# Performance work log

Measured on AMD Instinct MI355X. Metric: run time of the kernel, lower is better.

## Reference

```python
import jax, jax.numpy as jnp
import numpy as np

N, E = 50000, 300000
IN, HID, OUT, HEADS = 768, 256, 128, 8
RELS = ("writes", "written_by", "cites")


def setup_inputs():
    ks = iter(jax.random.split(jax.random.key(0), 64))

    def nrm(shape, scale=1.0):
        return jax.random.normal(next(ks), shape, dtype=jnp.float32) * scale

    inp = {"x_paper": nrm((N, IN)), "x_author": nrm((N, IN))}
    for name in ("ei_writes", "ei_written_by", "ei_cites"):
        inp[name] = jax.random.randint(next(ks), (2, E), 0, N, dtype=jnp.int32)
    # layer 0: in=IN, out=HID, heads=HEADS
    s0 = 1.0 / np.sqrt(IN)
    inp["W0_paper"] = nrm((IN, HID), s0); inp["b0_paper"] = jnp.zeros((HID,), jnp.float32)
    inp["W0_author"] = nrm((IN, HID), s0); inp["b0_author"] = jnp.zeros((HID,), jnp.float32)
    D0 = HID // HEADS
    for rel in RELS:
        inp["a0s_" + rel] = nrm((HEADS, D0), 0.1)
        inp["a0d_" + rel] = nrm((HEADS, D0), 0.1)
    inp["Wk0"] = nrm((HID, HID), 1.0 / np.sqrt(HID)); inp["bk0"] = jnp.zeros((HID,), jnp.float32)
    inp["q0"] = nrm((HID,), 0.1)
    # layer 1 (last): in=HID, out=OUT, heads=1
    s1 = 1.0 / np.sqrt(HID)
    inp["W1_paper"] = nrm((HID, OUT), s1); inp["b1_paper"] = jnp.zeros((OUT,), jnp.float32)
    inp["W1_author"] = nrm((HID, OUT), s1); inp["b1_author"] = jnp.zeros((OUT,), jnp.float32)
    for rel in RELS:
        inp["a1s_" + rel] = nrm((1, OUT), 0.1)
        inp["a1d_" + rel] = nrm((1, OUT), 0.1)
    inp["Wk1"] = nrm((OUT, OUT), 1.0 / np.sqrt(OUT)); inp["bk1"] = jnp.zeros((OUT,), jnp.float32)
    inp["q1"] = nrm((OUT,), 0.1)
    return inp


def _han_layer(xs, proj, att, Wk, bk, q, edges, heads):
    # xs: {ntype: [N, in]}, proj: {ntype: (W, b)}, att: {rel: (a_src[H,D], a_dst[H,D])}
    C = q.shape[0]
    D = C // heads
    xh = {nt: (x @ proj[nt][0] + proj[nt][1]).reshape(-1, heads, D) for nt, x in xs.items()}
    outs = {nt: [] for nt in xs}
    for (st, rel, dt), ei in edges:
        a_s, a_d = att[rel]
        xsrc, xdst = xh[st], xh[dt]
        src, dst = ei[0], ei[1]
        n = xdst.shape[0]
        # GAT-style edge scores per head: [E, H]
        al = jax.nn.leaky_relu((xsrc * a_s).sum(-1)[src] + (xdst * a_d).sum(-1)[dst], 0.2)
        amax = jax.lax.stop_gradient(jax.ops.segment_max(al, dst, num_segments=n))
        ex = jnp.exp(al - amax[dst])
        alpha = ex / (jax.ops.segment_sum(ex, dst, num_segments=n)[dst] + 1e-16)
        msg = xsrc[src] * alpha[:, :, None]                      # [E, H, D]
        agg = jax.ops.segment_sum(msg, dst, num_segments=n)      # [n, H, D]
        outs[dt].append(jax.nn.relu(agg.reshape(n, C)))
    # semantic attention across metapaths (group)
    res = {}
    for nt, lst in outs.items():
        stk = jnp.stack(lst)                                     # [M, n, C]
        score = (q * jnp.tanh(stk @ Wk + bk).mean(axis=1)).sum(-1)
        w = jax.nn.softmax(score)                                # [M]
        res[nt] = jnp.einsum('m,mnc->nc', w, stk)
    return res


def reference(x_paper, x_author, W0_paper, b0_paper, W0_author, b0_author,
              a0s_writes, a0d_writes, a0s_written_by, a0d_written_by, a0s_cites, a0d_cites,
              Wk0, bk0, q0,
              W1_paper, b1_paper, W1_author, b1_author,
              a1s_writes, a1d_writes, a1s_written_by, a1d_written_by, a1s_cites, a1d_cites,
              Wk1, bk1, q1,
              ei_writes, ei_written_by, ei_cites):
    edges = [(("author", "writes", "paper"), ei_writes),
             (("paper", "written_by", "author"), ei_written_by),
             (("paper", "cites", "paper"), ei_cites)]
    h = _han_layer({"paper": x_paper, "author": x_author},
                   {"paper": (W0_paper, b0_paper), "author": (W0_author, b0_author)},
                   {"writes": (a0s_writes, a0d_writes),
                    "written_by": (a0s_written_by, a0d_written_by),
                    "cites": (a0s_cites, a0d_cites)},
                   Wk0, bk0, q0, edges, HEADS)
    h = {k: jax.nn.elu(v) for k, v in h.items()}
    h = _han_layer(h,
                   {"paper": (W1_paper, b1_paper), "author": (W1_author, b1_author)},
                   {"writes": (a1s_writes, a1d_writes),
                    "written_by": (a1s_written_by, a1d_written_by),
                    "cites": (a1s_cites, a1d_cites)},
                   Wk1, bk1, q1, edges, 1)

    def l2n(v):
        return v / jnp.maximum(jnp.linalg.norm(v, axis=1, keepdims=True), 1e-12)

    return (l2n(h["paper"]), l2n(h["author"]))
```

## Files before the change

### kernel.cpp

```cpp
#include <hip/hip_runtime.h>
#include <math.h>

#define NN 50000
#define NE 300000
#define DIN 768
#define DHID 256
#define DOUT 128
#define H0 8
#define D0 32
#define OFFST (NN + 4)

typedef __attribute__((ext_vector_type(8))) short bf16x8;
typedef __attribute__((ext_vector_type(8))) unsigned short u16x8;
typedef __attribute__((ext_vector_type(4))) float f32x4;

__device__ __forceinline__ unsigned short f2bf(float f) {
    unsigned u = __float_as_uint(f);
    unsigned r = (u + 0x7fffu + ((u >> 16) & 1u)) >> 16;
    return (unsigned short)r;
}
__device__ __forceinline__ float bf2f(unsigned short u) {
    return __uint_as_float(((unsigned)u) << 16);
}

__device__ __forceinline__ void gload16(const void* g, void* l) {
    __builtin_amdgcn_global_load_lds(
        (const __attribute__((address_space(1))) unsigned int*)g,
        (__attribute__((address_space(3))) unsigned int*)l, 16, 0, 0);
}

__device__ __forceinline__ void store_bf8(unsigned short* dst, float4 lo, float4 hi) {
    u16x8 o;
    o[0] = f2bf(lo.x); o[1] = f2bf(lo.y); o[2] = f2bf(lo.z); o[3] = f2bf(lo.w);
    o[4] = f2bf(hi.x); o[5] = f2bf(hi.y); o[6] = f2bf(hi.z); o[7] = f2bf(hi.w);
    *(u16x8*)dst = o;
}

__global__ void transconv3_kernel(const float* __restrict__ Wa, const float* __restrict__ Wb,
                                  const float* __restrict__ Wc,
                                  unsigned short* __restrict__ Ta, unsigned short* __restrict__ Tb,
                                  unsigned short* __restrict__ Tc,
                                  int Kab, int Nab, int Kc, int Ncc)
{
    int y = blockIdx.y;
    const float* W = (y == 0) ? Wa : ((y == 1) ? Wb : Wc);
    unsigned short* T = (y == 0) ? Ta : ((y == 1) ? Tb : Tc);
    int K = (y == 2) ? Kc : Kab;
    int Nc = (y == 2) ? Ncc : Nab;
    int gid = blockIdx.x * 256 + threadIdx.x;
    if (gid >= K * Nc) return;
    int k = gid / Nc, n = gid - k * Nc;
    T[(size_t)n * K + k] = f2bf(W[gid]);
}

__global__ __launch_bounds__(512) void gemm_l0_kernel(
    const float* __restrict__ A0, const float* __restrict__ A1,
    const unsigned short* __restrict__ Bt0, const unsigned short* __restrict__ Bt1,
    const float* __restrict__ bias0, const float* __restrict__ bias1,
    unsigned short* __restrict__ C0, unsigned short* __restrict__ C1)
{
    constexpr int K  = DIN;
    constexpr int Nc = DHID;
    constexpr int NT = K / 32;
    __shared__ __align__(16) unsigned short As[2][128 * 32];
    __shared__ __align__(16) unsigned short Bs[2][256 * 32];
    const int z = blockIdx.y;
    const float* A = z ? A1 : A0;
    const unsigned short* Bt = z ? Bt1 : Bt0;
    const float* bias = z ? bias1 : bias0;
    unsigned short* C = z ? C1 : C0;
    const int t = threadIdx.x;
    const int lane = t & 63, w = t >> 6;
    const int wr = w >> 2, wc = w & 3;
    const int bm = blockIdx.x * 128;

    f32x4 acc[4][4];
    #pragma unroll
    for (int m = 0; m < 4; ++m)
        #pragma unroll
        for (int n = 0; n < 4; ++n)
            acc[m][n] = (f32x4){0.f, 0.f, 0.f, 0.f};

    const int arow = t >> 2;
    const int ags = (t & 3) ^ ((arow >> 1) & 3);
    int ar = bm + arow; if (ar >= NN) ar = NN - 1;
    const float* pA = A + (size_t)ar * K + ags * 8;
    const int b0row = t >> 2;
    const int bg0 = (t & 3) ^ ((b0row >> 1) & 3);
    const unsigned short* pB0 = Bt + (size_t)b0row * K + bg0 * 8;
    const int c1i = t + 512;
    const int b1row = c1i >> 2;
    const int bg1 = (c1i & 3) ^ ((b1row >> 1) & 3);
    const unsigned short* pB1 = Bt + (size_t)b1row * K + bg1 * 8;

    const int rA = wr * 64 + (lane & 15);
    const int rB = wc * 64 + (lane & 15);
    const int gw = lane >> 4;

    float4 ra[2][2];
    {
        float4 t0 = *(const float4*)(pA);
        float4 t1 = *(const float4*)(pA + 4);
        gload16(pB0, &Bs[0][(size_t)t * 8]);
        gload16(pB1, &Bs[0][(size_t)c1i * 8]);
        ra[1][0] = *(const float4*)(pA + 32);
        ra[1][1] = *(const float4*)(pA + 36);
        gload16(pB0 + 32, &Bs[1][(size_t)t * 8]);
        gload16(pB1 + 32, &Bs[1][(size_t)c1i * 8]);
        store_bf8(&As[0][(size_t)t * 8], t0, t1);
    }
    asm volatile("s_waitcnt vmcnt(4) lgkmcnt(0)\n\ts_barrier" ::: "memory");

    #pragma unroll
    for (int ti = 0; ti < NT; ++ti) {
        const int cur = ti & 1;
        const int nxt = cur ^ 1;
        if (ti + 1 < NT) {
            const int nk = (ti + 1) * 32;
            gload16(pB0 + nk, &Bs[nxt][(size_t)t * 8]);
            gload16(pB1 + nk, &Bs[nxt][(size_t)c1i * 8]);
        }
        if (ti + 2 < NT) {
            const int nk = (ti + 2) * 32;
            ra[cur][0] = *(const float4*)(pA + nk);
            ra[cur][1] = *(const float4*)(pA + nk + 4);
        }
        bf16x8 afr[4], bfr[4];
        #pragma unroll
        for (int m = 0; m < 4; ++m) {
            int r = rA + m * 16;
            afr[m] = *(const bf16x8*)&As[cur][r * 32 + ((gw ^ ((r >> 1) & 3)) * 8)];
        }
        #pragma unroll
        for (int n = 0; n < 4; ++n) {
            int r = rB + n * 16;
            bfr[n] = *(const bf16x8*)&Bs[cur][r * 32 + ((gw ^ ((r >> 1) & 3)) * 8)];
        }
        #pragma unroll
        for (int m = 0; m < 4; ++m)
            #pragma unroll
            for (int n = 0; n < 4; ++n)
                acc[m][n] = __builtin_amdgcn_mfma_f32_16x16x32_bf16(afr[m], bfr[n], acc[m][n], 0, 0, 0);
        if (ti + 1 < NT) {
            store_bf8(&As[nxt][(size_t)t * 8], ra[nxt][0], ra[nxt][1]);
            if (ti + 2 < NT) asm volatile("s_waitcnt vmcnt(2) lgkmcnt(0)\n\ts_barrier" ::: "memory");
            else             asm volatile("s_waitcnt vmcnt(0) lgkmcnt(0)\n\ts_barrier" ::: "memory");
        }
    }

    #pragma unroll
    for (int m = 0; m < 4; ++m) {
        #pragma unroll
        for (int j = 0; j < 4; ++j) {
            int row = bm + wr * 64 + m * 16 + (lane >> 4) * 4 + j;
            if (row >= NN) continue;
            #pragma unroll
            for (int n = 0; n < 4; ++n) {
                int col = wc * 64 + n * 16 + (lane & 15);
                C[(size_t)row * Nc + col] = f2bf(acc[m][n][j] + bias[col]);
            }
        }
    }
}

__global__ __launch_bounds__(256) void gemm_bf16_kernel(
    const unsigned short* __restrict__ A0, const unsigned short* __restrict__ A1,
    const unsigned short* __restrict__ Bt0, const unsigned short* __restrict__ Bt1,
    const float* __restrict__ bias0, const float* __restrict__ bias1,
    unsigned short* __restrict__ C0, unsigned short* __restrict__ C1,
    int M, int K, int Nc)
{
    __shared__ __align__(16) unsigned short As[2][128 * 32];
    __shared__ __align__(16) unsigned short Bs[2][128 * 32];
    const int z = blockIdx.z;
    const unsigned short* A  = z ? A1  : A0;
    const unsigned short* Bt = z ? Bt1 : Bt0;
    const float* bias = z ? bias1 : bias0;
    unsigned short* C = z ? C1 : C0;
    const int t = threadIdx.x;
    const int lane = t & 63, w = t >> 6;
    const int wr = w >> 1, wc = w & 1;
    const int bm = blockIdx.y * 128, bn = blockIdx.x * 128;

    f32x4 acc[4][4];
    #pragma unroll
    for (int m = 0; m < 4; ++m)
        #pragma unroll
        for (int n = 0; n < 4; ++n)
            acc[m][n] = (f32x4){0.f, 0.f, 0.f, 0.f};

    const int c0 = w * 64 + lane, c1 = c0 + 256;
    const int row0 = c0 >> 2, row1 = c1 >> 2;
    const int g0 = (c0 & 3) ^ ((row0 >> 1) & 3);
    const int g1 = (c1 & 3) ^ ((row1 >> 1) & 3);
    const int ar0 = (bm + row0 < M) ? (bm + row0) : (M - 1);
    const int ar1 = (bm + row1 < M) ? (bm + row1) : (M - 1);
    const unsigned short* pA0 = A + (size_t)ar0 * K + g0 * 8;
    const unsigned short* pA1 = A + (size_t)ar1 * K + g1 * 8;
    const unsigned short* pB0 = Bt + (size_t)(bn + row0) * K + g0 * 8;
    const unsigned short* pB1 = Bt + (size_t)(bn + row1) * K + g1 * 8;

    const int rA = wr * 64 + (lane & 15);
    const int rB = wc * 64 + (lane & 15);
    const int gw = lane >> 4;
    const int nt = K >> 5;

    gload16(pA0, &As[0][c0 * 8]);
    gload16(pA1, &As[0][c1 * 8]);
    gload16(pB0, &Bs[0][c0 * 8]);
    gload16(pB1, &Bs[0][c1 * 8]);
    __syncthreads();
    for (int ti = 0; ti < nt; ++ti) {
        const int cur = ti & 1;
        if (ti + 1 < nt) {
            const int nk = (ti + 1) << 5;
            const int nb = cur ^ 1;
            gload16(pA0 + nk, &As[nb][c0 * 8]);
            gload16(pA1 + nk, &As[nb][c1 * 8]);
            gload16(pB0 + nk, &Bs[nb][c0 * 8]);
            gload16(pB1 + nk, &Bs[nb][c1 * 8]);
        }
        bf16x8 afr[4], bfr[4];
        #pragma unroll
        for (int m = 0; m < 4; ++m) {
            int r = rA + m * 16;
            afr[m] = *(const bf16x8*)&As[cur][r * 32 + ((gw ^ ((r >> 1) & 3)) * 8)];
        }
        #pragma unroll
        for (int n = 0; n < 4; ++n) {
            int r = rB + n * 16;
            bfr[n] = *(const bf16x8*)&Bs[cur][r * 32 + ((gw ^ ((r >> 1) & 3)) * 8)];
        }
        #pragma unroll
        for (int m = 0; m < 4; ++m)
            #pragma unroll
            for (int n = 0; n < 4; ++n)
                acc[m][n] = __builtin_amdgcn_mfma_f32_16x16x32_bf16(afr[m], bfr[n], acc[m][n], 0, 0, 0);
        __syncthreads();
    }
    #pragma unroll
    for (int m = 0; m < 4; ++m) {
        #pragma unroll
        for (int j = 0; j < 4; ++j) {
            int row = bm + wr * 64 + m * 16 + (lane >> 4) * 4 + j;
            if (row >= M) continue;
            #pragma unroll
            for (int n = 0; n < 4; ++n) {
                int col = bn + wc * 64 + n * 16 + (lane & 15);
                C[(size_t)row * Nc + col] = f2bf(acc[m][n][j] + bias[col]);
            }
        }
    }
}

__global__ __launch_bounds__(256) void sem2_bf16_kernel(
    const unsigned short* __restrict__ Aa, const unsigned short* __restrict__ Ab,
    const unsigned short* __restrict__ Bt,
    const float* __restrict__ bk, float* __restrict__ partial0,
    int M, int K, int Nc)
{
    __shared__ __align__(16) unsigned short As[2][128 * 32];
    __shared__ __align__(16) unsigned short Bs[2][128 * 32];
    __shared__ float red[128];
    const int z = blockIdx.z;
    const unsigned short* A = z ? Ab : Aa;
    float* partial = partial0 + z * Nc;
    const int t = threadIdx.x;
    const int lane = t & 63, w = t >> 6;
    const int wr = w >> 1, wc = w & 1;
    const int bm = blockIdx.y * 128, bn = blockIdx.x * 128;

    f32x4 acc[4][4];
    #pragma unroll
    for (int m = 0; m < 4; ++m)
        #pragma unroll
        for (int n = 0; n < 4; ++n)
            acc[m][n] = (f32x4){0.f, 0.f, 0.f, 0.f};

    const int c0 = w * 64 + lane, c1 = c0 + 256;
    const int row0 = c0 >> 2, row1 = c1 >> 2;
    const int g0 = (c0 & 3) ^ ((row0 >> 1) & 3);
    const int g1 = (c1 & 3) ^ ((row1 >> 1) & 3);
    const int ar0 = (bm + row0 < M) ? (bm + row0) : (M - 1);
    const int ar1 = (bm + row1 < M) ? (bm + row1) : (M - 1);
    const unsigned short* pA0 = A + (size_t)ar0 * K + g0 * 8;
    const unsigned short* pA1 = A + (size_t)ar1 * K + g1 * 8;
    const unsigned short* pB0 = Bt + (size_t)(bn + row0) * K + g0 * 8;
    const unsigned short* pB1 = Bt + (size_t)(bn + row1) * K + g1 * 8;

    const int rA = wr * 64 + (lane & 15);
    const int rB = wc * 64 + (lane & 15);
    const int gw = lane >> 4;
    const int nt = K >> 5;

    gload16(pA0, &As[0][c0 * 8]);
    gload16(pA1, &As[0][c1 * 8]);
    gload16(pB0, &Bs[0][c0 * 8]);
    gload16(pB1, &Bs[0][c1 * 8]);
    __syncthreads();
    for (int ti = 0; ti < nt; ++ti) {
        const int cur = ti & 1;
        if (ti + 1 < nt) {
            const int nk = (ti + 1) << 5;
            const int nb = cur ^ 1;
            gload16(pA0 + nk, &As[nb][c0 * 8]);
            gload16(pA1 + nk, &As[nb][c1 * 8]);
            gload16(pB0 + nk, &Bs[nb][c0 * 8]);
            gload16(pB1 + nk, &Bs[nb][c1 * 8]);
        }
        bf16x8 afr[4], bfr[4];
        #pragma unroll
        for (int m = 0; m < 4; ++m) {
            int r = rA + m * 16;
            afr[m] = *(const bf16x8*)&As[cur][r * 32 + ((gw ^ ((r >> 1) & 3)) * 8)];
        }
        #pragma unroll
        for (int n = 0; n < 4; ++n) {
            int r = rB + n * 16;
            bfr[n] = *(const bf16x8*)&Bs[cur][r * 32 + ((gw ^ ((r >> 1) & 3)) * 8)];
        }
        #pragma unroll
        for (int m = 0; m < 4; ++m)
            #pragma unroll
            for (int n = 0; n < 4; ++n)
                acc[m][n] = __builtin_amdgcn_mfma_f32_16x16x32_bf16(afr[m], bfr[n], acc[m][n], 0, 0, 0);
        __syncthreads();
    }
    if (t < 128) red[t] = 0.f;
    __syncthreads();
    #pragma unroll
    for (int n = 0; n < 4; ++n) {
        int lcol = wc * 64 + n * 16 + (lane & 15);
        float b = bk[bn + lcol];
        float s = 0.f;
        #pragma unroll
        for (int m = 0; m < 4; ++m) {
            #pragma unroll
            for (int j = 0; j < 4; ++j) {
                int row = bm + wr * 64 + m * 16 + (lane >> 4) * 4 + j;
                if (row < M) s += tanhf(acc[m][n][j] + b);
            }
        }
        atomicAdd(&red[lcol], s);
    }
    __syncthreads();
    if (t < 128) atomicAdd(&partial[bn + t], red[t]);
}

__global__ void hist3_kernel(const int* __restrict__ d0, const int* __restrict__ d1,
                             const int* __restrict__ d2, int* __restrict__ deg3)
{
    int gid = blockIdx.x * 256 + threadIdx.x;
    if (gid >= 3 * NE) return;
    int rel = gid / NE, e = gid - rel * NE;
    const int* dst = (rel == 0) ? d0 : ((rel == 1) ? d1 : d2);
    atomicAdd(&deg3[rel * NN + dst[e]], 1);
}

__global__ void block_sum3_kernel(const int* __restrict__ deg3, int* __restrict__ bsum3)
{
    __shared__ int buf[256];
    int rel = blockIdx.y;
    int i = blockIdx.x * 256 + threadIdx.x;
    buf[threadIdx.x] = (i < NN) ? deg3[rel * NN + i] : 0;
    __syncthreads();
    for (int s = 128; s > 0; s >>= 1) {
        if (threadIdx.x < s) buf[threadIdx.x] += buf[threadIdx.x + s];
        __syncthreads();
    }
    if (threadIdx.x == 0) bsum3[rel * 256 + blockIdx.x] = buf[0];
}

__global__ void scan_bsum3_kernel(const int* __restrict__ bsum3, int* __restrict__ boff3, int nb)
{
    __shared__ int buf[256];
    int rel = blockIdx.y;
    int tid = threadIdx.x;
    int v = (tid < nb) ? bsum3[rel * 256 + tid] : 0;
    buf[tid] = v;
    __syncthreads();
    for (int off = 1; off < 256; off <<= 1) {
        int t = (tid >= off) ? buf[tid - off] : 0;
        __syncthreads();
        buf[tid] += t;
        __syncthreads();
    }
    if (tid < nb) boff3[rel * 256 + tid] = buf[tid] - v;
}

__global__ void scan_final3_kernel(const int* __restrict__ deg3, const int* __restrict__ boff3,
                                   int* __restrict__ offs3)
{
    __shared__ int buf[256];
    int rel = blockIdx.y;
    int tid = threadIdx.x, b = blockIdx.x;
    int i = b * 256 + tid;
    int v = (i < NN) ? deg3[rel * NN + i] : 0;
    buf[tid] = v;
    __syncthreads();
    for (int off = 1; off < 256; off <<= 1) {
        int t = (tid >= off) ? buf[tid - off] : 0;
        __syncthreads();
        buf[tid] += t;
        __syncthreads();
    }
    int* offs = offs3 + rel * OFFST;
    if (i < NN) offs[i] = boff3[rel * 256 + b] + buf[tid] - v;
    if (i == NN - 1) offs[NN] = boff3[rel * 256 + b] + buf[tid];
}

__global__ void place3_kernel(const int* __restrict__ s0, const int* __restrict__ s1,
                              const int* __restrict__ s2,
                              const int* __restrict__ offs3, int* __restrict__ cnt3,
                              int* __restrict__ esrc3)
{
    int rel = blockIdx.y;
    int e = blockIdx.x * 256 + threadIdx.x;
    if (e >= NE) return;
    const int* srcdst = (rel == 0) ? s0 : ((rel == 1) ? s1 : s2);
    int src = srcdst[e];
    int d = srcdst[NE + e];
    int p = offs3[rel * OFFST + d] + atomicAdd(&cnt3[rel * NN + d], 1);
    esrc3[rel * NE + p] = src;
}

__global__ void scores_L0_kernel(
    const unsigned short* __restrict__ xp, const unsigned short* __restrict__ xa,
    const float* __restrict__ a_dw, const float* __restrict__ a_swb,
    const float* __restrict__ a_sc, const float* __restrict__ a_dc,
    const float* __restrict__ a_sw, const float* __restrict__ a_dwb,
    float* __restrict__ sW_dst, float* __restrict__ sWB_src,
    float* __restrict__ sC_src, float* __restrict__ sC_dst,
    float* __restrict__ sW_src, float* __restrict__ sWB_dst)
{
    int gid = blockIdx.x * 256 + threadIdx.x;
    int half = NN * H0;
    if (gid >= 2 * half) return;
    if (gid < half) {
        int node = gid >> 3, h = gid & 7;
        const unsigned short* xr = xp + (size_t)node * DHID + h * D0;
        float xv[D0];
        #pragma unroll
        for (int j = 0; j < 4; ++j) {
            u16x8 v = ((const u16x8*)xr)[j];
            #pragma unroll
            for (int k = 0; k < 8; ++k) xv[j * 8 + k] = bf2f(v[k]);
        }
        const float* p0 = a_dw  + h * D0;
        const float* p1 = a_swb + h * D0;
        const float* p2 = a_sc  + h * D0;
        const float* p3 = a_dc  + h * D0;
        float d0 = 0.f, d1 = 0.f, d2 = 0.f, d3 = 0.f;
        #pragma unroll
        for (int k = 0; k < D0; ++k) {
            float x = xv[k];
            d0 += x * p0[k]; d1 += x * p1[k]; d2 += x * p2[k]; d3 += x * p3[k];
        }
        sW_dst[gid] = d0; sWB_src[gid] = d1; sC_src[gid] = d2; sC_dst[gid] = d3;
    } else {
        int g = gid - half;
        int node = g >> 3, h = g & 7;
        const unsigned short* xr = xa + (size_t)node * DHID + h * D0;
        float xv[D0];
        #pragma unroll
        for (int j = 0; j < 4; ++j) {
            u16x8 v = ((const u16x8*)xr)[j];
            #pragma unroll
            for (int k = 0; k < 8; ++k) xv[j * 8 + k] = bf2f(v[k]);
        }
        const float* p0 = a_sw  + h * D0;
        const float* p1 = a_dwb + h * D0;
        float d0 = 0.f, d1 = 0.f;
        #pragma unroll
        for (int k = 0; k < D0; ++k) {
            float x = xv[k];
            d0 += x * p0[k]; d1 += x * p1[k];
        }
        sW_src[g] = d0; sWB_dst[g] = d1;
    }
}

__global__ void scores_L1_kernel(
    const unsigned short* __restrict__ xp, const unsigned short* __restrict__ xa,
    const float* __restrict__ a_dw, const float* __restrict__ a_swb,
    const float* __restrict__ a_sc, const float* __restrict__ a_dc,
    const float* __restrict__ a_sw, const float* __restrict__ a_dwb,
    float* __restrict__ sW_dst, float* __restrict__ sWB_src,
    float* __restrict__ sC_src, float* __restrict__ sC_dst,
    float* __restrict__ sW_src, float* __restrict__ sWB_dst)
{
    int gid = blockIdx.x * 256 + threadIdx.x;
    if (gid >= 2 * NN) return;
    if (gid < NN) {
        const unsigned short* xr = xp + (size_t)gid * DOUT;
        float d0 = 0.f, d1 = 0.f, d2 = 0.f, d3 = 0.f;
        for (int j = 0; j < DOUT / 8; ++j) {
            u16x8 v = ((const u16x8*)xr)[j];
            #pragma unroll
            for (int k = 0; k < 8; ++k) {
                float x = bf2f(v[k]);
                int c = j * 8 + k;
                d0 += x * a_dw[c]; d1 += x * a_swb[c]; d2 += x * a_sc[c]; d3 += x * a_dc[c];
            }
        }
        sW_dst[gid] = d0; sWB_src[gid] = d1; sC_src[gid] = d2; sC_dst[gid] = d3;
    } else {
        int g = gid - NN;
        const unsigned short* xr = xa + (size_t)g * DOUT;
        float d0 = 0.f, d1 = 0.f;
        for (int j = 0; j < DOUT / 8; ++j) {
            u16x8 v = ((const u16x8*)xr)[j];
            #pragma unroll
            for (int k = 0; k < 8; ++k) {
                float x = bf2f(v[k]);
                int c = j * 8 + k;
                d0 += x * a_sw[c]; d1 += x * a_dwb[c];
            }
        }
        sW_src[g] = d0; sWB_dst[g] = d1;
    }
}

__global__ void seg_alpha3_kernel(
    const int* __restrict__ offs3, const int* __restrict__ esrc3,
    const float* __restrict__ ss0, const float* __restrict__ ss1, const float* __restrict__ ss2,
    const float* __restrict__ sd0, const float* __restrict__ sd1, const float* __restrict__ sd2,
    float* __restrict__ alpha3, int H)
{
    int rel = blockIdx.y;
    const int* offs = offs3 + rel * OFFST;
    const int* esrc = esrc3 + rel * NE;
    const float* ssrc = (rel == 0) ? ss0 : ((rel == 1) ? ss1 : ss2);
    const float* sdst = (rel == 0) ? sd0 : ((rel == 1) ? sd1 : sd2);
    float* alpha = alpha3 + (size_t)rel * NE * H0;
    int gid = blockIdx.x * 256 + threadIdx.x;
    if (gid >= NN * H) return;
    int d = gid / H, h = gid - d * H;
    int beg = offs[d], end = offs[d + 1];
    float sd = sdst[gid];
    float m = -INFINITY, den = 0.f;
    for (int i = beg; i < end; ++i) {
        int s = esrc[i];
        float v = ssrc[s * H + h] + sd;
        v = (v >= 0.f) ? v : 0.2f * v;
        if (v > m) { den = den * expf(m - v) + 1.f; m = v; }
        else       den += expf(v - m);
    }
    float inv = 1.f / (den + 1e-16f);
    for (int i = beg; i < end; ++i) {
        int s = esrc[i];
        float v = ssrc[s * H + h] + sd;
        v = (v >= 0.f) ? v : 0.2f * v;
        alpha[(size_t)i * H + h] = expf(v - m) * inv;
    }
}

template<int CPL, int HH, int DSH>
__global__ __launch_bounds__(256) void gather3_kernel(
    const int* __restrict__ offs3, const int* __restrict__ esrc3,
    const float* __restrict__ alpha3,
    const unsigned short* __restrict__ x0, const unsigned short* __restrict__ x1,
    const unsigned short* __restrict__ x2,
    unsigned short* __restrict__ o0, unsigned short* __restrict__ o1,
    unsigned short* __restrict__ o2, int C)
{
    int rel = blockIdx.y;
    const int* offs = offs3 + rel * OFFST;
    const int* esrc = esrc3 + rel * NE;
    const float* alpha = alpha3 + (size_t)rel * NE * H0;
    const unsigned short* x = (rel == 0) ? x0 : ((rel == 1) ? x1 : x2);
    unsigned short* outp = (rel == 0) ? o0 : ((rel == 1) ? o1 : o2);

    int wid = threadIdx.x >> 6, lane = threadIdx.x & 63;
    int d = blockIdx.x * 4 + wid;
    int c0 = lane * CPL;
    int h = c0 >> DSH;
    int beg = offs[d], end = offs[d + 1];
    float acc0 = 0.f, acc1 = 0.f, acc2 = 0.f, acc3 = 0.f;
    int n = end - beg;
    if (n > 0) {
        int sA = esrc[beg];
        float aA = alpha[(size_t)beg * HH + h];
        int sB = sA; float aB = 0.f;
        if (n > 1) { sB = esrc[beg + 1]; aB = alpha[(size_t)(beg + 1) * HH + h]; }
        if (CPL == 4) {
            ushort4 xc = *(const ushort4*)(x + (size_t)sA * C + c0);
            for (int i = beg; i < end; ++i) {
                ushort4 xn = xc;
                if (i + 1 < end) xn = *(const ushort4*)(x + (size_t)sB * C + c0);
                int sN = sB; float aN = 0.f;
                if (i + 2 < end) { sN = esrc[i + 2]; aN = alpha[(size_t)(i + 2) * HH + h]; }
                acc0 += aA * bf2f(xc.x); acc1 += aA * bf2f(xc.y);
                acc2 += aA * bf2f(xc.z); acc3 += aA * bf2f(xc.w);
                xc = xn; aA = aB; sB = sN; aB = aN;
            }
        } else {
            ushort2 xc = *(const ushort2*)(x + (size_t)sA * C + c0);
            for (int i = beg; i < end; ++i) {
                ushort2 xn = xc;
                if (i + 1 < end) xn = *(const ushort2*)(x + (size_t)sB * C + c0);
                int sN = sB; float aN = 0.f;
                if (i + 2 < end) { sN = esrc[i + 2]; aN = alpha[(size_t)(i + 2) * HH + h]; }
                acc0 += aA * bf2f(xc.x); acc1 += aA * bf2f(xc.y);
                xc = xn; aA = aB; sB = sN; aB = aN;
            }
        }
    }
    unsigned short* op = outp + (size_t)d * C + c0;
    if (CPL == 4) {
        ushort4 st;
        st.x = f2bf(fmaxf(acc0, 0.f)); st.y = f2bf(fmaxf(acc1, 0.f));
        st.z = f2bf(fmaxf(acc2, 0.f)); st.w = f2bf(fmaxf(acc3, 0.f));
        *(ushort4*)op = st;
    } else {
        ushort2 st;
        st.x = f2bf(fmaxf(acc0, 0.f)); st.y = f2bf(fmaxf(acc1, 0.f));
        *(ushort2*)op = st;
    }
}

__global__ void sem_weights_kernel(const float* __restrict__ partial, const float* __restrict__ q,
                                   float* __restrict__ w, int C, int n)
{
    if (threadIdx.x != 0 || blockIdx.x != 0) return;
    float inv = 1.f / (float)n;
    float s0 = 0.f, s1 = 0.f;
    for (int c = 0; c < C; ++c) {
        s0 += q[c] * partial[c] * inv;
        s1 += q[c] * partial[C + c] * inv;
    }
    float m = fmaxf(s0, s1);
    float e0 = expf(s0 - m), e1 = expf(s1 - m);
    float den = e0 + e1;
    w[0] = e0 / den;
    w[1] = e1 / den;
}

__global__ void combine2_bf16_kernel(const unsigned short* __restrict__ a,
                                     const unsigned short* __restrict__ b,
                                     const float* __restrict__ w, unsigned short* __restrict__ out,
                                     int n8)
{
    int i = blockIdx.x * 256 + threadIdx.x;
    if (i >= n8) return;
    float w0 = w[0], w1 = w[1];
    u16x8 va = ((const u16x8*)a)[i];
    u16x8 vb = ((const u16x8*)b)[i];
    u16x8 o;
    #pragma unroll
    for (int j = 0; j < 8; ++j) o[j] = f2bf(w0 * bf2f(va[j]) + w1 * bf2f(vb[j]));
    ((u16x8*)out)[i] = o;
}

__global__ __launch_bounds__(128) void final_norm_kernel(
    const unsigned short* __restrict__ aggW, const unsigned short* __restrict__ aggC,
    const unsigned short* __restrict__ aggB, const float* __restrict__ w,
    float* __restrict__ out)
{
    __shared__ float red[128];
    int row = blockIdx.x;
    int c = threadIdx.x;
    float v;
    if (row < NN) {
        size_t i = (size_t)row * DOUT + c;
        v = w[0] * bf2f(aggW[i]) + w[1] * bf2f(aggC[i]);
    } else {
        size_t i = (size_t)(row - NN) * DOUT + c;
        v = bf2f(aggB[i]);
    }
    red[c] = v * v;
    __syncthreads();
    for (int s = 64; s > 0; s >>= 1) {
        if (c < s) red[c] += red[c + s];
        __syncthreads();
    }
    float norm = sqrtf(red[0]);
    out[(size_t)row * DOUT + c] = v / fmaxf(norm, 1e-12f);
}

extern "C" void kernel_launch(void* const* d_in, const int* in_sizes, int n_in,
                              void* d_out, int out_size, void* d_ws, size_t ws_size,
                              hipStream_t stream)
{
    const float* x_paper   = (const float*)d_in[0];
    const float* x_author  = (const float*)d_in[1];
    const int*   ei_writes = (const int*)d_in[2];
    const int*   ei_wb     = (const int*)d_in[3];
    const int*   ei_cites  = (const int*)d_in[4];
    const float* W0p = (const float*)d_in[5];  const float* b0p = (const float*)d_in[6];
    const float* W0a = (const float*)d_in[7];  const float* b0a = (const float*)d_in[8];
    const float* a0s_w  = (const float*)d_in[9];  const float* a0d_w  = (const float*)d_in[10];
    const float* a0s_wb = (const float*)d_in[11]; const float* a0d_wb = (const float*)d_in[12];
    const float* a0s_c  = (const float*)d_in[13]; const float* a0d_c  = (const float*)d_in[14];
    const float* Wk0 = (const float*)d_in[15]; const float* bk0 = (const float*)d_in[16];
    const float* q0  = (const float*)d_in[17];
    const float* W1p = (const float*)d_in[18]; const float* b1p = (const float*)d_in[19];
    const float* W1a = (const float*)d_in[20]; const float* b1a = (const float*)d_in[21];
    const float* a1s_w  = (const float*)d_in[22]; const float* a1d_w  = (const float*)d_in[23];
    const float* a1s_wb = (const float*)d_in[24]; const float* a1d_wb = (const float*)d_in[25];
    const float* a1s_c  = (const float*)d_in[26]; const float* a1d_c  = (const float*)d_in[27];
    const float* Wk1 = (const float*)d_in[28]; const float* bk1 = (const float*)d_in[29];
    const float* q1  = (const float*)d_in[30];

    float* out = (float*)d_out;

    const size_t NH = (size_t)NN * DHID;
    const size_t NI = (size_t)NN * DIN;
    const size_t NO = (size_t)NN * DOUT;
    const size_t NH2 = NH * 2;
    const size_t NI2 = NI * 2;
    const size_t NO2 = NO * 2;

    char* base = (char*)d_ws;
    unsigned short* xbhP = (unsigned short*)(base + 0);
    unsigned short* xbhA = (unsigned short*)(base + NH2);
    unsigned short* aggW = (unsigned short*)(base + 2 * NH2);
    unsigned short* aggC = (unsigned short*)(base + 3 * NH2);
    unsigned short* aggB = (unsigned short*)(base + 4 * NH2);
    unsigned short* hbP  = (unsigned short*)(base + 0);
    unsigned short* hbA  = aggB;
    unsigned short* x1Pb = (unsigned short*)(base + NH2);
    unsigned short* x1Ab = (unsigned short*)(base + NH2 + NO2);
    unsigned short* agg1W = (unsigned short*)(base + 2 * NH2 + NI2);
    unsigned short* agg1C = (unsigned short*)(base + 2 * NH2 + NI2 + NO2);
    unsigned short* agg1B = (unsigned short*)(base + 2 * NH2 + NI2 + 2 * NO2);

    float* sW_src  = (float*)(base + 204800000);
    float* sW_dst  = sW_src  + NN * H0;
    float* sWB_src = sW_dst  + NN * H0;
    float* sWB_dst = sWB_src + NN * H0;
    float* sC_src  = sWB_dst + NN * H0;
    float* sC_dst  = sC_src  + NN * H0;
    float* alpha3  = (float*)(base + 214400000);
    int* ip     = (int*)(base + 243200000);
    int* offs3  = ip;  ip += 3 * OFFST;
    int* esrc3  = ip;  ip += 3 * NE;
    int* deg3   = ip;  ip += 3 * NN;
    int* bsum3  = ip;  ip += 3 * 256;
    int* boff3  = ip;  ip += 3 * 256;
    unsigned short* wt0p = (unsigned short*)ip;
    unsigned short* wt0a = wt0p + (size_t)DHID * DIN;
    unsigned short* wkt  = wt0a + (size_t)DHID * DIN;
    unsigned short* wt1p = wt0p;
    unsigned short* wt1a = wt1p + (size_t)DOUT * DHID;
    float* tsum = (float*)(wkt + (size_t)DHID * DHID);
    float* wsem = tsum + 512;

    const int NB = (NN + 255) / 256;

    hipMemsetAsync(deg3, 0, 3 * NN * sizeof(int), stream);
    hist3_kernel<<<(3 * NE + 255) / 256, 256, 0, stream>>>(ei_writes + NE, ei_wb + NE, ei_cites + NE, deg3);
    block_sum3_kernel<<<dim3(NB, 3), 256, 0, stream>>>(deg3, bsum3);
    scan_bsum3_kernel<<<dim3(1, 3), 256, 0, stream>>>(bsum3, boff3, NB);
    scan_final3_kernel<<<dim3(NB, 3), 256, 0, stream>>>(deg3, boff3, offs3);
    hipMemsetAsync(deg3, 0, 3 * NN * sizeof(int), stream);
    place3_kernel<<<dim3((NE + 255) / 256, 3), 256, 0, stream>>>(ei_writes, ei_wb, ei_cites, offs3, deg3, esrc3);

    hipMemsetAsync(tsum, 0, 512 * sizeof(float), stream);
    transconv3_kernel<<<dim3((DIN * DHID + 255) / 256, 3), 256, 0, stream>>>(
        W0p, W0a, Wk0, wt0p, wt0a, wkt, DIN, DHID, DHID, DHID);

    dim3 g0((NN + 127) / 128, 2);
    gemm_l0_kernel<<<g0, 512, 0, stream>>>(x_paper, x_author, wt0p, wt0a, b0p, b0a, xbhP, xbhA);

    scores_L0_kernel<<<(2 * NN * H0 + 255) / 256, 256, 0, stream>>>(
        xbhP, xbhA, a0d_w, a0s_wb, a0s_c, a0d_c, a0s_w, a0d_wb,
        sW_dst, sWB_src, sC_src, sC_dst, sW_src, sWB_dst);
    dim3 ga0((NN * H0 + 255) / 256, 3);
    seg_alpha3_kernel<<<ga0, 256, 0, stream>>>(
        offs3, esrc3, sW_src, sWB_src, sC_src, sW_dst, sWB_dst, sC_dst, alpha3, H0);
    dim3 gg0(NN / 4, 3);
    gather3_kernel<4, H0, 5><<<gg0, 256, 0, stream>>>(
        offs3, esrc3, alpha3, xbhA, xbhP, xbhP, aggW, aggB, aggC, DHID);

    dim3 gs0(DHID / 128, (NN + 127) / 128, 2);
    sem2_bf16_kernel<<<gs0, 256, 0, stream>>>(aggW, aggC, wkt, bk0, tsum, NN, DHID, DHID);
    sem_weights_kernel<<<1, 64, 0, stream>>>(tsum, q0, wsem, DHID, NN);

    combine2_bf16_kernel<<<(int)((NH / 8 + 255) / 256), 256, 0, stream>>>(aggW, aggC, wsem, hbP, (int)(NH / 8));

    transconv3_kernel<<<dim3((DHID * DOUT + 255) / 256, 3), 256, 0, stream>>>(
        W1p, W1a, Wk1, wt1p, wt1a, wkt, DHID, DOUT, DOUT, DOUT);

    dim3 g1(DOUT / 128, (NN + 127) / 128, 2);
    gemm_bf16_kernel<<<g1, 256, 0, stream>>>(hbP, hbA, wt1p, wt1a, b1p, b1a, x1Pb, x1Ab, NN, DHID, DOUT);

    hipMemsetAsync(tsum, 0, 2 * DOUT * sizeof(float), stream);

    scores_L1_kernel<<<(2 * NN + 255) / 256, 256, 0, stream>>>(
        x1Pb, x1Ab, a1d_w, a1s_wb, a1s_c, a1d_c, a1s_w, a1d_wb,
        sW_dst, sWB_src, sC_src, sC_dst, sW_src, sWB_dst);
    dim3 ga1((NN + 255) / 256, 3);
    seg_alpha3_kernel<<<ga1, 256, 0, stream>>>(
        offs3, esrc3, sW_src, sWB_src, sC_src, sW_dst, sWB_dst, sC_dst, alpha3, 1);
    dim3 gg1(NN / 4, 3);
    gather3_kernel<2, 1, 7><<<gg1, 256, 0, stream>>>(
        offs3, esrc3, alpha3, x1Ab, x1Pb, x1Pb, agg1W, agg1B, agg1C, DOUT);

    dim3 gs1(DOUT / 128, (NN + 127) / 128, 2);
    sem2_bf16_kernel<<<gs1, 256, 0, stream>>>(agg1W, agg1C, wkt, bk1, tsum, NN, DOUT, DOUT);
    sem_weights_kernel<<<1, 64, 0, stream>>>(tsum, q1, wsem, DOUT, NN);

    final_norm_kernel<<<2 * NN, 128, 0, stream>>>(agg1W, agg1C, agg1B, wsem, out);
}
```

Baseline: 728.0 us.

## Split layer-0 GEMM into 128-column tiles with triple-buffered B prefetch

The layer-0 projection GEMM now uses a 128x128 output tile per block instead of 128x256, so the grid gains a column dimension and each block handles half the output columns. B tiles move to a three-stage shared-memory ring prefetched two steps ahead, matching the A register prefetch depth. The goal is more blocks for better occupancy and latency hiding, and smaller shared-memory and register use per block. The cost is that each block loads its fp32 A rows and converts them to bf16 twice, once per column half, which doubles A global traffic.

```diff
diff --git a/kernel.cpp b/kernel.cpp
--- a/kernel.cpp
+++ b/kernel.cpp
@@ -63,8 +63,8 @@
     constexpr int Nc = DHID;
     constexpr int NT = K / 32;
     __shared__ __align__(16) unsigned short As[2][128 * 32];
-    __shared__ __align__(16) unsigned short Bs[2][256 * 32];
-    const int z = blockIdx.y;
+    __shared__ __align__(16) unsigned short Bs[3][128 * 32];
+    const int z = blockIdx.z;
     const float* A = z ? A1 : A0;
     const unsigned short* Bt = z ? Bt1 : Bt0;
     const float* bias = z ? bias1 : bias0;
@@ -72,78 +72,68 @@
     const int t = threadIdx.x;
     const int lane = t & 63, w = t >> 6;
     const int wr = w >> 2, wc = w & 3;
-    const int bm = blockIdx.x * 128;
-
-    f32x4 acc[4][4];
+    const int bm = blockIdx.y * 128, bn = blockIdx.x * 128;
+
+    f32x4 acc[4][2];
     #pragma unroll
     for (int m = 0; m < 4; ++m)
         #pragma unroll
-        for (int n = 0; n < 4; ++n)
+        for (int n = 0; n < 2; ++n)
             acc[m][n] = (f32x4){0.f, 0.f, 0.f, 0.f};
 
     const int arow = t >> 2;
     const int ags = (t & 3) ^ ((arow >> 1) & 3);
     int ar = bm + arow; if (ar >= NN) ar = NN - 1;
     const float* pA = A + (size_t)ar * K + ags * 8;
-    const int b0row = t >> 2;
-    const int bg0 = (t & 3) ^ ((b0row >> 1) & 3);
-    const unsigned short* pB0 = Bt + (size_t)b0row * K + bg0 * 8;
-    const int c1i = t + 512;
-    const int b1row = c1i >> 2;
-    const int bg1 = (c1i & 3) ^ ((b1row >> 1) & 3);
-    const unsigned short* pB1 = Bt + (size_t)b1row * K + bg1 * 8;
+    const int brow = t >> 2;
+    const int bgs = (t & 3) ^ ((brow >> 1) & 3);
+    const unsigned short* pB = Bt + (size_t)(bn + brow) * K + bgs * 8;
 
     const int rA = wr * 64 + (lane & 15);
-    const int rB = wc * 64 + (lane & 15);
+    const int rB = wc * 32 + (lane & 15);
     const int gw = lane >> 4;
 
     float4 ra[2][2];
     {
         float4 t0 = *(const float4*)(pA);
         float4 t1 = *(const float4*)(pA + 4);
-        gload16(pB0, &Bs[0][(size_t)t * 8]);
-        gload16(pB1, &Bs[0][(size_t)c1i * 8]);
+        gload16(pB, &Bs[0][(size_t)t * 8]);
         ra[1][0] = *(const float4*)(pA + 32);
         ra[1][1] = *(const float4*)(pA + 36);
-        gload16(pB0 + 32, &Bs[1][(size_t)t * 8]);
-        gload16(pB1 + 32, &Bs[1][(size_t)c1i * 8]);
+        gload16(pB + 32, &Bs[1][(size_t)t * 8]);
         store_bf8(&As[0][(size_t)t * 8], t0, t1);
     }
-    asm volatile("s_waitcnt vmcnt(4) lgkmcnt(0)\n\ts_barrier" ::: "memory");
+    asm volatile("s_waitcnt vmcnt(3) lgkmcnt(0)\n\ts_barrier" ::: "memory");
 
     #pragma unroll
     for (int ti = 0; ti < NT; ++ti) {
-        const int cur = ti & 1;
-        const int nxt = cur ^ 1;
-        if (ti + 1 < NT) {
-            const int nk = (ti + 1) * 32;
-            gload16(pB0 + nk, &Bs[nxt][(size_t)t * 8]);
-            gload16(pB1 + nk, &Bs[nxt][(size_t)c1i * 8]);
-        }
+        const int rcv = ti & 1;
+        const int con = rcv ^ 1;
         if (ti + 2 < NT) {
             const int nk = (ti + 2) * 32;
-            ra[cur][0] = *(const float4*)(pA + nk);
-            ra[cur][1] = *(const float4*)(pA + nk + 4);
-        }
-        bf16x8 afr[4], bfr[4];
+            ra[rcv][0] = *(const float4*)(pA + nk);
+            ra[rcv][1] = *(const float4*)(pA + nk + 4);
+            gload16(pB + nk, &Bs[(ti + 2) % 3][(size_t)t * 8]);
+        }
+        bf16x8 afr[4], bfr[2];
         #pragma unroll
         for (int m = 0; m < 4; ++m) {
             int r = rA + m * 16;
-            afr[m] = *(const bf16x8*)&As[cur][r * 32 + ((gw ^ ((r >> 1) & 3)) * 8)];
-        }
-        #pragma unroll
-        for (int n = 0; n < 4; ++n) {
+            afr[m] = *(const bf16x8*)&As[rcv][r * 32 + ((gw ^ ((r >> 1) & 3)) * 8)];
+        }
+        #pragma unroll
+        for (int n = 0; n < 2; ++n) {
             int r = rB + n * 16;
-            bfr[n] = *(const bf16x8*)&Bs[cur][r * 32 + ((gw ^ ((r >> 1) & 3)) * 8)];
+            bfr[n] = *(const bf16x8*)&Bs[ti % 3][r * 32 + ((gw ^ ((r >> 1) & 3)) * 8)];
         }
         #pragma unroll
         for (int m = 0; m < 4; ++m)
             #pragma unroll
-            for (int n = 0; n < 4; ++n)
+            for (int n = 0; n < 2; ++n)
                 acc[m][n] = __builtin_amdgcn_mfma_f32_16x16x32_bf16(afr[m], bfr[n], acc[m][n], 0, 0, 0);
         if (ti + 1 < NT) {
-            store_bf8(&As[nxt][(size_t)t * 8], ra[nxt][0], ra[nxt][1]);
-            if (ti + 2 < NT) asm volatile("s_waitcnt vmcnt(2) lgkmcnt(0)\n\ts_barrier" ::: "memory");
+            store_bf8(&As[con][(size_t)t * 8], ra[con][0], ra[con][1]);
+            if (ti + 2 < NT) asm volatile("s_waitcnt vmcnt(3) lgkmcnt(0)\n\ts_barrier" ::: "memory");
             else             asm volatile("s_waitcnt vmcnt(0) lgkmcnt(0)\n\ts_barrier" ::: "memory");
         }
     }
@@ -155,8 +145,8 @@
             int row = bm + wr * 64 + m * 16 + (lane >> 4) * 4 + j;
             if (row >= NN) continue;
             #pragma unroll
-            for (int n = 0; n < 4; ++n) {
-                int col = wc * 64 + n * 16 + (lane & 15);
+            for (int n = 0; n < 2; ++n) {
+                int col = bn + wc * 32 + n * 16 + (lane & 15);
                 C[(size_t)row * Nc + col] = f2bf(acc[m][n][j] + bias[col]);
             }
         }
@@ -760,7 +750,7 @@
     transconv3_kernel<<<dim3((DIN * DHID + 255) / 256, 3), 256, 0, stream>>>(
         W0p, W0a, Wk0, wt0p, wt0a, wkt, DIN, DHID, DHID, DHID);
 
-    dim3 g0((NN + 127) / 128, 2);
+    dim3 g0(DHID / 128, (NN + 127) / 128, 2);
     gemm_l0_kernel<<<g0, 512, 0, stream>>>(x_paper, x_author, wt0p, wt0a, b0p, b0a, xbhP, xbhA);
 
     scores_L0_kernel<<<(2 * NN * H0 + 255) / 256, 256, 0, stream>>>(
```

Result: no change. 719.6 us (-1.2%).
